# Performance work log

Hardware: AMD Instinct MI355X
Metric: run time of the kernel (lower is better)

The kernel has to match this reference:

```python
import jax, jax.numpy as jnp
import numpy as np

EMBED_DIM = 1024
NUM_HEADS = 16
HEAD_DIM = EMBED_DIM // NUM_HEADS
SCALE = HEAD_DIM ** -0.5


def setup_inputs() -> dict:
    key = jax.random.key(0)
    k_x, k_wqkv, k_bqkv, k_wp, k_bp = jax.random.split(key, 5)
    B, N = 2, 2048
    x = jax.random.normal(k_x, (B, N, EMBED_DIM), dtype=jnp.float32)
    # torch.nn.Linear default init: U(-1/sqrt(fan_in), 1/sqrt(fan_in))
    lim = 1.0 / np.sqrt(EMBED_DIM)
    W_qkv = jax.random.uniform(k_wqkv, (EMBED_DIM, 3 * EMBED_DIM), jnp.float32, -lim, lim)
    b_qkv = jax.random.uniform(k_bqkv, (3 * EMBED_DIM,), jnp.float32, -lim, lim)
    W_proj = jax.random.uniform(k_wp, (EMBED_DIM, EMBED_DIM), jnp.float32, -lim, lim)
    b_proj = jax.random.uniform(k_bp, (EMBED_DIM,), jnp.float32, -lim, lim)
    return {"x": x, "W_qkv": W_qkv, "b_qkv": b_qkv, "W_proj": W_proj, "b_proj": b_proj}


def reference(x, W_qkv, b_qkv, W_proj, b_proj):
    B, N, C = x.shape
    qkv = x @ W_qkv + b_qkv                              # [B, N, 3C]
    qkv = qkv.reshape(B, N, 3, NUM_HEADS, HEAD_DIM)
    qkv = jnp.transpose(qkv, (2, 0, 3, 1, 4))            # [3, B, H, N, D]
    q, k, v = qkv[0], qkv[1], qkv[2]
    attn = jnp.einsum('bhnd,bhmd->bhnm', q, k) * SCALE   # [B, H, N, N]
    attn = jax.nn.softmax(attn, axis=-1)
    out = jnp.einsum('bhnm,bhmd->bhnd', attn, v)         # [B, H, N, D]
    out = jnp.transpose(out, (0, 2, 1, 3)).reshape(B, N, C)
    return out @ W_proj + b_proj
```

## Files before the change

### kernel.cpp

```cpp
#include <hip/hip_runtime.h>
#include <math.h>

typedef unsigned short u16;
typedef _Float16 f16;
typedef f16 f16x8 __attribute__((ext_vector_type(8)));
typedef __fp16 hp16x2 __attribute__((ext_vector_type(2)));
typedef float f32x4 __attribute__((ext_vector_type(4)));
typedef float f32x16 __attribute__((ext_vector_type(16)));
typedef unsigned u32x2 __attribute__((ext_vector_type(2)));

#define SEQ   2048
#define NH    16
#define HD    64
#define EMB   1024
#define NQKV  3072
#define BATCH 2
#define QSCALE 0.18033688f

__device__ __forceinline__ u16 f2h(float f) {
  union { f16 h; u16 u; } w; w.h = (f16)f; return w.u;
}

__device__ __forceinline__ void gload16(const void* g, void* l) {
  __builtin_amdgcn_global_load_lds(
      (const __attribute__((address_space(1))) unsigned int*)g,
      (__attribute__((address_space(3))) unsigned int*)l, 16, 0, 0);
}

__device__ __forceinline__ void cvt_wt_tile(const float* __restrict__ W,
                                            u16* __restrict__ Wt,
                                            int K, int N, int n0, int k0, int t) {
  __shared__ u16 T[64][68];
  const int rr = t >> 4, cc = (t & 15) << 2;
#pragma unroll
  for (int p = 0; p < 4; p++) {
    const int kr = p * 16 + rr;
    float4 v = *reinterpret_cast<const float4*>(&W[(size_t)(k0 + kr) * N + n0 + cc]);
    T[cc + 0][kr] = f2h(v.x); T[cc + 1][kr] = f2h(v.y);
    T[cc + 2][kr] = f2h(v.z); T[cc + 3][kr] = f2h(v.w);
  }
  __syncthreads();
#pragma unroll
  for (int p = 0; p < 4; p++) {
    const int nr = p * 16 + rr;
    union { u16 s[4]; unsigned long long d; } o;
    o.s[0] = T[nr][cc + 0]; o.s[1] = T[nr][cc + 1];
    o.s[2] = T[nr][cc + 2]; o.s[3] = T[nr][cc + 3];
    *reinterpret_cast<unsigned long long*>(&Wt[(size_t)(n0 + nr) * K + k0 + cc]) = o.d;
  }
}

__global__ __launch_bounds__(256) void k_pre(const float* __restrict__ X,
                                             u16* __restrict__ Xh,
                                             const float* __restrict__ Wqkv,
                                             u16* __restrict__ Wt,
                                             const float* __restrict__ Wproj,
                                             u16* __restrict__ Wpt) {
  const int b = blockIdx.x;
  const int t = threadIdx.x;
  if (b < 2048) {
    const size_t i = ((size_t)b * 256 + t) * 8;
    float4 a = *reinterpret_cast<const float4*>(&X[i]);
    float4 c = *reinterpret_cast<const float4*>(&X[i + 4]);
    union { hp16x2 h2[4]; float4 f; } pk;
    pk.h2[0] = __builtin_amdgcn_cvt_pkrtz(a.x, a.y);
    pk.h2[1] = __builtin_amdgcn_cvt_pkrtz(a.z, a.w);
    pk.h2[2] = __builtin_amdgcn_cvt_pkrtz(c.x, c.y);
    pk.h2[3] = __builtin_amdgcn_cvt_pkrtz(c.z, c.w);
    *reinterpret_cast<float4*>(&Xh[i]) = pk.f;
  } else if (b < 2048 + 768) {
    const int id = b - 2048;
    cvt_wt_tile(Wqkv, Wt, EMB, NQKV, (id % 48) << 6, (id / 48) << 6, t);
  } else {
    const int id = b - 2816;
    cvt_wt_tile(Wproj, Wpt, EMB, EMB, (id % 16) << 6, (id / 16) << 6, t);
  }
}

__device__ __forceinline__ void gemm_core_sb(const u16* __restrict__ Ag,
                                             const u16* __restrict__ Bg,
                                             int m0, int n0, int t,
                                             f32x4 acc[4][4]) {
  __shared__ __align__(16) u16 As[128 * 32];
  __shared__ __align__(16) u16 Bs[128 * 32];
  const int lane = t & 63, w = t >> 6;
  const int l15  = lane & 15, quad = lane >> 4;
  const int wm = w >> 1, wn = w & 1;
  const int srow  = lane >> 2;
  const int gslot = (lane & 3) ^ ((srow >> 1) & 3);
  const int xk    = (quad ^ ((l15 >> 1) & 3)) << 3;

  for (int k0 = 0; k0 < EMB; k0 += 32) {
    __syncthreads();
#pragma unroll
    for (int i = 0; i < 2; i++) {
      const int ca = w * 2 + i;
      const int arow = ca * 16 + srow;
      gload16(Ag + (size_t)(m0 + arow) * EMB + k0 + gslot * 8, &As[ca * 512]);
      gload16(Bg + (size_t)(n0 + arow) * EMB + k0 + gslot * 8, &Bs[ca * 512]);
    }
    __syncthreads();
    f16x8 af[4], bf[4];
#pragma unroll
    for (int s = 0; s < 4; s++)
      af[s] = *reinterpret_cast<const f16x8*>(&As[(wm * 64 + s * 16 + l15) * 32 + xk]);
#pragma unroll
    for (int s = 0; s < 4; s++)
      bf[s] = *reinterpret_cast<const f16x8*>(&Bs[(wn * 64 + s * 16 + l15) * 32 + xk]);
#pragma unroll
    for (int i = 0; i < 4; i++)
#pragma unroll
      for (int j = 0; j < 4; j++)
        acc[i][j] = __builtin_amdgcn_mfma_f32_16x16x32_f16(af[i], bf[j], acc[i][j], 0, 0, 0);
  }
}

__global__ __launch_bounds__(128, 2) void k_qkv(const u16* __restrict__ Ag,
                                                const u16* __restrict__ Bg,
                                                const float* __restrict__ bias,
                                                u16* __restrict__ qo,
                                                u16* __restrict__ ko,
                                                u16* __restrict__ vo) {
  __shared__ __align__(16) u16 SM[4][128 * 32];
  const int t = threadIdx.x;
  const int lane = t & 63, w = t >> 6;
  const int l15 = lane & 15, quad = lane >> 4;
  const int srow  = lane >> 2;
  const int gslot = (lane & 3) ^ ((srow >> 1) & 3);
  const int xk    = (quad ^ ((l15 >> 1) & 3)) << 3;
  const int id  = blockIdx.y * 24 + blockIdx.x;
  const int xcd = id & 7, rr = id >> 3;
  const int n_t = 12 * (xcd & 1) + rr % 12;
  const int m_t = 8 * (xcd >> 1) + rr / 12;
  const int m0 = m_t << 7, n0 = n_t << 7;

  f32x4 acc[4][8];
#pragma unroll
  for (int i = 0; i < 4; i++)
#pragma unroll
    for (int j = 0; j < 8; j++) acc[i][j] = (f32x4){0.f, 0.f, 0.f, 0.f};

  auto STAGE = [&](int buf, int k0) {
#pragma unroll
    for (int i = 0; i < 4; i++) {
      const int ca = w * 4 + i;
      const int arow = ca * 16 + srow;
      gload16(Ag + (size_t)(m0 + arow) * EMB + k0 + gslot * 8, &SM[buf][ca * 512]);
      gload16(Bg + (size_t)(n0 + arow) * EMB + k0 + gslot * 8, &SM[2 + buf][ca * 512]);
    }
  };

  STAGE(0, 0);
  __syncthreads();

  for (int kt = 0; kt < 32; ++kt) {
    if (kt + 1 < 32) STAGE((kt + 1) & 1, (kt + 1) * 32);
    const u16* Asb = SM[kt & 1];
    const u16* Bsb = SM[2 + (kt & 1)];
    f16x8 af[4], bf[8];
#pragma unroll
    for (int s = 0; s < 4; s++)
      af[s] = *reinterpret_cast<const f16x8*>(
          &Asb[(w * 64 + s * 16 + l15) * 32 + xk]);
#pragma unroll
    for (int s = 0; s < 8; s++)
      bf[s] = *reinterpret_cast<const f16x8*>(
          &Bsb[(s * 16 + l15) * 32 + xk]);
    __builtin_amdgcn_s_setprio(1);
#pragma unroll
    for (int i = 0; i < 4; i++)
#pragma unroll
      for (int j = 0; j < 8; j++)
        acc[i][j] = __builtin_amdgcn_mfma_f32_16x16x32_f16(af[i], bf[j],
                                                           acc[i][j], 0, 0, 0);
    __builtin_amdgcn_s_setprio(0);
    __syncthreads();
  }

  if (n0 >= 2048) {
    u16* T = &SM[0][0];
#pragma unroll
    for (int j = 0; j < 8; j++) {
      const int c  = n0 + j * 16 + l15;
      const float bv = bias[c];
      const int dl = j * 16 + l15;
#pragma unroll
      for (int i = 0; i < 4; i++) {
#pragma unroll
        for (int r2 = 0; r2 < 4; r2++) {
          const int ml = w * 64 + i * 16 + quad * 4 + r2;
          T[dl * 128 + ((((ml >> 3) ^ (dl & 15)) << 3) | (ml & 7))] =
              f2h(acc[i][j][r2] + bv);
        }
      }
    }
    __syncthreads();
    const int bb = m0 >> 11, nb = m0 & (SEQ - 1);
    const int cg = lane & 15;
#pragma unroll
    for (int it = 0; it < 16; ++it) {
      const int row = w * 64 + it * 4 + (lane >> 4);
      union { f16x8 v; float4 f; } u;
      u.v = *reinterpret_cast<const f16x8*>(
          &T[row * 128 + ((cg ^ (row & 15)) << 3)]);
      const int c = n0 + row;
      const int h = (c >> 6) & 15, d = c & 63;
      *reinterpret_cast<float4*>(
          &vo[((size_t)(bb * NH + h) * HD + d) * SEQ + nb + cg * 8]) = u.f;
    }
  } else {
#pragma unroll
    for (int j = 0; j < 8; j++) {
      const int c = n0 + j * 16 + l15;
      const int which = c >> 10, h = (c >> 6) & 15, d = c & 63;
      const float bv = bias[c];
      const float sc = (which == 0) ? QSCALE : 1.0f;
#pragma unroll
      for (int i = 0; i < 4; i++) {
#pragma unroll
        for (int r2 = 0; r2 < 4; r2++) {
          const int m  = m0 + w * 64 + i * 16 + quad * 4 + r2;
          const int bb = m >> 11, n = m & (SEQ - 1);
          const u16 val = f2h((acc[i][j][r2] + bv) * sc);
          if (which == 1)
            ko[((((size_t)bb * NH + h) * SEQ) + n) * HD + d] = val;
          else
            qo[((((size_t)bb * NH + h) * SEQ) + n) * HD + d] = val;
        }
      }
    }
  }
}

__global__ __launch_bounds__(256) void k_proj(const u16* __restrict__ Ag,
                                              const u16* __restrict__ Bg,
                                              const float* __restrict__ bias,
                                              float* __restrict__ out) {
  const int t = threadIdx.x;
  const int lane = t & 63, w = t >> 6;
  const int l15 = lane & 15, quad = lane >> 4;
  const int wm = w >> 1, wn = w & 1;
  const int m0 = blockIdx.y << 7, n0 = blockIdx.x << 7;
  f32x4 acc[4][4];
#pragma unroll
  for (int i = 0; i < 4; i++)
#pragma unroll
    for (int j = 0; j < 4; j++) acc[i][j] = (f32x4){0.f, 0.f, 0.f, 0.f};
  gemm_core_sb(Ag, Bg, m0, n0, t, acc);
#pragma unroll
  for (int j = 0; j < 4; j++) {
    const int c = n0 + wn * 64 + j * 16 + l15;
    const float bv = bias[c];
#pragma unroll
    for (int i = 0; i < 4; i++) {
#pragma unroll
      for (int r2 = 0; r2 < 4; r2++) {
        const int m = m0 + wm * 64 + i * 16 + quad * 4 + r2;
        out[(size_t)m * EMB + c] = acc[i][j][r2] + bv;
      }
    }
  }
}

__global__ __launch_bounds__(512, 4) void k_attn(const u16* __restrict__ Qg,
                                                 const u16* __restrict__ Kg,
                                                 const u16* __restrict__ Vtg,
                                                 u16* __restrict__ AO) {
  __shared__ __align__(16) u16 KV[2][2][2][64 * 64];
  __shared__ float Lx[256];
  const int t    = threadIdx.x;
  const int lane = t & 63, w = t >> 6;
  const int grp  = w >> 2, wl = w & 3;
  const int l31  = lane & 31, hi = lane >> 5;
  const int id   = blockIdx.y * 16 + blockIdx.x;
  const int swz  = ((id & 7) << 6) | (id >> 3);
  const int bh   = swz >> 4;
  const int q0   = (swz & 15) << 7;
  const size_t base = (size_t)bh * SEQ * HD;

  f16x8 qf[4];
  {
    const u16* qp = Qg + base + (size_t)(q0 + 32 * wl + l31) * HD + hi * 8;
#pragma unroll
    for (int c = 0; c < 4; c++) {
      union { float4 f; f16x8 v; } fu;
      fu.f = *reinterpret_cast<const float4*>(qp + c * 16);
      qf[c] = fu.v;
    }
  }

  f32x16 O0 = {}, O1 = {};
  float lsum = 0.f;
  const int fsw = (l31 >> 1) & 7;
  const int srw = lane >> 3, ssl = lane & 7;
  const int kbeg = grp << 10;
  const int kend = kbeg + (SEQ / 2);

  auto STAGE = [&](int buf, int kt) {
    u16* Ksb = KV[buf][grp][0];
    u16* Vsb = KV[buf][grp][1];
#pragma unroll
    for (int i = 0; i < 2; i++) {
      const int ca  = wl * 2 + i;
      const int row = ca * 8 + srw;
      const int sg  = (ssl ^ ((row >> 1) & 7)) << 3;
      gload16(Kg  + base + (size_t)(kt + row) * HD + sg, &Ksb[ca * 512]);
      gload16(Vtg + base + (size_t)row * SEQ + kt + sg,  &Vsb[ca * 512]);
    }
  };

  STAGE(0, kbeg);
  __syncthreads();

  int cur = 0;
  for (int kt = kbeg; kt < kend; kt += 64) {
    if (kt + 64 < kend) STAGE(cur ^ 1, kt + 64);
    const u16* Ks = KV[cur][grp][0];
    const u16* Vs = KV[cur][grp][1];

#pragma unroll
    for (int sk = 0; sk < 2; sk++) {
      f32x16 c = {};
      __builtin_amdgcn_s_setprio(1);
#pragma unroll
      for (int cc = 0; cc < 4; cc++) {
        f16x8 kf = *reinterpret_cast<const f16x8*>(
            &Ks[(sk * 32 + l31) * 64 + (((cc * 2 + hi) ^ fsw) << 3)]);
        c = __builtin_amdgcn_mfma_f32_32x32x16_f16(kf, qf[cc], c, 0, 0, 0);
      }
      __builtin_amdgcn_s_setprio(0);
      unsigned pw[4][2];
#pragma unroll
      for (int g = 0; g < 4; g++) {
        const float p0 = __builtin_amdgcn_exp2f(c[4 * g + 0]);
        const float p1 = __builtin_amdgcn_exp2f(c[4 * g + 1]);
        const float p2 = __builtin_amdgcn_exp2f(c[4 * g + 2]);
        const float p3 = __builtin_amdgcn_exp2f(c[4 * g + 3]);
        lsum += (p0 + p1) + (p2 + p3);
        union { hp16x2 h; unsigned u; } w0, w1;
        w0.h = __builtin_amdgcn_cvt_pkrtz(p0, p1);
        w1.h = __builtin_amdgcn_cvt_pkrtz(p2, p3);
        pw[g][0] = w0.u; pw[g][1] = w1.u;
      }
      __builtin_amdgcn_s_setprio(1);
#pragma unroll
      for (int s = 0; s < 2; s++) {
        u32x2 r02 = __builtin_amdgcn_permlane32_swap(
            pw[2 * s][0], pw[2 * s + 1][0], false, false);
        u32x2 r13 = __builtin_amdgcn_permlane32_swap(
            pw[2 * s][1], pw[2 * s + 1][1], false, false);
        union { unsigned u[4]; f16x8 v; } fr;
        fr.u[0] = r02.x;
        fr.u[1] = r13.x;
        fr.u[2] = r02.y;
        fr.u[3] = r13.y;
        const int cc = sk * 2 + s;
        f16x8 vf0 = *reinterpret_cast<const f16x8*>(
            &Vs[l31 * 64 + (((cc * 2 + hi) ^ fsw) << 3)]);
        f16x8 vf1 = *reinterpret_cast<const f16x8*>(
            &Vs[(32 + l31) * 64 + (((cc * 2 + hi) ^ fsw) << 3)]);
        O0 = __builtin_amdgcn_mfma_f32_32x32x16_f16(fr.v, vf0, O0, 0, 0, 0);
        O1 = __builtin_amdgcn_mfma_f32_32x32x16_f16(fr.v, vf1, O1, 0, 0, 0);
      }
      __builtin_amdgcn_s_setprio(0);
    }
    __syncthreads();
    cur ^= 1;
  }

  float* Xch = reinterpret_cast<float*>(&KV[0][0][0][0]);
  const int li = wl * 64 + lane;
  if (grp == 1) {
#pragma unroll
    for (int g4 = 0; g4 < 4; g4++) {
      f32x4 v0 = { O0[4 * g4 + 0], O0[4 * g4 + 1], O0[4 * g4 + 2], O0[4 * g4 + 3] };
      *reinterpret_cast<f32x4*>(&Xch[(g4 * 256 + li) * 4]) = v0;
      f32x4 v1 = { O1[4 * g4 + 0], O1[4 * g4 + 1], O1[4 * g4 + 2], O1[4 * g4 + 3] };
      *reinterpret_cast<f32x4*>(&Xch[((4 + g4) * 256 + li) * 4]) = v1;
    }
    Lx[li] = lsum;
  }
  __syncthreads();
  if (grp == 0) {
#pragma unroll
    for (int g4 = 0; g4 < 4; g4++) {
      f32x4 v0 = *reinterpret_cast<const f32x4*>(&Xch[(g4 * 256 + li) * 4]);
      f32x4 v1 = *reinterpret_cast<const f32x4*>(&Xch[((4 + g4) * 256 + li) * 4]);
#pragma unroll
      for (int j = 0; j < 4; j++) {
        O0[4 * g4 + j] += v0[j];
        O1[4 * g4 + j] += v1[j];
      }
    }
    lsum += Lx[li];
    lsum += __shfl_xor(lsum, 32);
    const int b = bh >> 4, h = bh & 15;
#pragma unroll
    for (int g = 0; g < 4; g++) {
#pragma unroll
      for (int rr = 0; rr < 4; rr++) {
        const int r = g * 4 + rr;
        const int qrow = rr + 8 * g + 4 * hi;
        const float inv = 1.f / __shfl(lsum, qrow, 64);
        const int n = q0 + 32 * wl + qrow;
        u16* dst = AO + ((size_t)(b * SEQ + n)) * EMB + h * HD;
        dst[l31]      = f2h(O0[r] * inv);
        dst[32 + l31] = f2h(O1[r] * inv);
      }
    }
  }
}

extern "C" void kernel_launch(void* const* d_in, const int* in_sizes, int n_in,
                              void* d_out, int out_size, void* d_ws, size_t ws_size,
                              hipStream_t stream) {
  (void)in_sizes; (void)n_in; (void)out_size; (void)ws_size;
  const float* x     = (const float*)d_in[0];
  const float* Wqkv  = (const float*)d_in[1];
  const float* bqkv  = (const float*)d_in[2];
  const float* Wproj = (const float*)d_in[3];
  const float* bproj = (const float*)d_in[4];
  float* out = (float*)d_out;

  const size_t NE = (size_t)BATCH * SEQ * EMB;
  u16* q    = (u16*)d_ws;
  u16* k    = q + NE;
  u16* vt   = k + NE;
  u16* aoxh = vt + NE;
  u16* Wt   = aoxh + NE;
  u16* Wpt  = Wt + (size_t)NQKV * EMB;

  k_pre<<<3072, 256, 0, stream>>>(x, aoxh, Wqkv, Wt, Wproj, Wpt);

  dim3 gq(NQKV / 128, (BATCH * SEQ) / 128);
  k_qkv<<<gq, 128, 0, stream>>>(aoxh, Wt, bqkv, q, k, vt);

  dim3 ga(SEQ / 128, BATCH * NH);
  k_attn<<<ga, 512, 0, stream>>>(q, k, vt, aoxh);

  dim3 gp(EMB / 128, (BATCH * SEQ) / 128);
  k_proj<<<gp, 256, 0, stream>>>(aoxh, Wpt, bproj, out);
}
```

Measured before the change: 187.2 us.

## Give each attention wave two 32-row query tiles, halving block size

```diff
diff --git a/kernel.cpp b/kernel.cpp
--- a/kernel.cpp
+++ b/kernel.cpp
@@ -262,15 +262,15 @@
   }
 }
 
-__global__ __launch_bounds__(512, 4) void k_attn(const u16* __restrict__ Qg,
-                                                 const u16* __restrict__ Kg,
-                                                 const u16* __restrict__ Vtg,
-                                                 u16* __restrict__ AO) {
+__global__ __launch_bounds__(256) void k_attn(const u16* __restrict__ Qg,
+                                              const u16* __restrict__ Kg,
+                                              const u16* __restrict__ Vtg,
+                                              u16* __restrict__ AO) {
   __shared__ __align__(16) u16 KV[2][2][2][64 * 64];
-  __shared__ float Lx[256];
+  __shared__ float Lx[2][128];
   const int t    = threadIdx.x;
   const int lane = t & 63, w = t >> 6;
-  const int grp  = w >> 2, wl = w & 3;
+  const int grp  = w >> 1, wl = w & 1;
   const int l31  = lane & 31, hi = lane >> 5;
   const int id   = blockIdx.y * 16 + blockIdx.x;
   const int swz  = ((id & 7) << 6) | (id >> 3);
@@ -278,19 +278,20 @@
   const int q0   = (swz & 15) << 7;
   const size_t base = (size_t)bh * SEQ * HD;
 
-  f16x8 qf[4];
-  {
-    const u16* qp = Qg + base + (size_t)(q0 + 32 * wl + l31) * HD + hi * 8;
+  f16x8 qf[2][4];
+#pragma unroll
+  for (int qs = 0; qs < 2; qs++) {
+    const u16* qp = Qg + base + (size_t)(q0 + 64 * wl + 32 * qs + l31) * HD + hi * 8;
 #pragma unroll
     for (int c = 0; c < 4; c++) {
       union { float4 f; f16x8 v; } fu;
       fu.f = *reinterpret_cast<const float4*>(qp + c * 16);
-      qf[c] = fu.v;
-    }
-  }
-
-  f32x16 O0 = {}, O1 = {};
-  float lsum = 0.f;
+      qf[qs][c] = fu.v;
+    }
+  }
+
+  f32x16 O[2][2] = {};
+  float lsum[2] = {0.f, 0.f};
   const int fsw = (l31 >> 1) & 7;
   const int srw = lane >> 3, ssl = lane & 7;
   const int kbeg = grp << 10;
@@ -300,8 +301,8 @@
     u16* Ksb = KV[buf][grp][0];
     u16* Vsb = KV[buf][grp][1];
 #pragma unroll
-    for (int i = 0; i < 2; i++) {
-      const int ca  = wl * 2 + i;
+    for (int i = 0; i < 4; i++) {
+      const int ca  = wl * 4 + i;
       const int row = ca * 8 + srw;
       const int sg  = (ssl ^ ((row >> 1) & 7)) << 3;
       gload16(Kg  + base + (size_t)(kt + row) * HD + sg, &Ksb[ca * 512]);
@@ -320,47 +321,54 @@
 
 #pragma unroll
     for (int sk = 0; sk < 2; sk++) {
-      f32x16 c = {};
+      f32x16 cq[2] = {};
       __builtin_amdgcn_s_setprio(1);
 #pragma unroll
       for (int cc = 0; cc < 4; cc++) {
         f16x8 kf = *reinterpret_cast<const f16x8*>(
             &Ks[(sk * 32 + l31) * 64 + (((cc * 2 + hi) ^ fsw) << 3)]);
-        c = __builtin_amdgcn_mfma_f32_32x32x16_f16(kf, qf[cc], c, 0, 0, 0);
+        cq[0] = __builtin_amdgcn_mfma_f32_32x32x16_f16(kf, qf[0][cc], cq[0], 0, 0, 0);
+        cq[1] = __builtin_amdgcn_mfma_f32_32x32x16_f16(kf, qf[1][cc], cq[1], 0, 0, 0);
       }
       __builtin_amdgcn_s_setprio(0);
-      unsigned pw[4][2];
-#pragma unroll
-      for (int g = 0; g < 4; g++) {
-        const float p0 = __builtin_amdgcn_exp2f(c[4 * g + 0]);
-        const float p1 = __builtin_amdgcn_exp2f(c[4 * g + 1]);
-        const float p2 = __builtin_amdgcn_exp2f(c[4 * g + 2]);
-        const float p3 = __builtin_amdgcn_exp2f(c[4 * g + 3]);
-        lsum += (p0 + p1) + (p2 + p3);
-        union { hp16x2 h; unsigned u; } w0, w1;
-        w0.h = __builtin_amdgcn_cvt_pkrtz(p0, p1);
-        w1.h = __builtin_amdgcn_cvt_pkrtz(p2, p3);
-        pw[g][0] = w0.u; pw[g][1] = w1.u;
+      unsigned pw[2][4][2];
+#pragma unroll
+      for (int qs = 0; qs < 2; qs++) {
+#pragma unroll
+        for (int g = 0; g < 4; g++) {
+          const float p0 = __builtin_amdgcn_exp2f(cq[qs][4 * g + 0]);
+          const float p1 = __builtin_amdgcn_exp2f(cq[qs][4 * g + 1]);
+          const float p2 = __builtin_amdgcn_exp2f(cq[qs][4 * g + 2]);
+          const float p3 = __builtin_amdgcn_exp2f(cq[qs][4 * g + 3]);
+          lsum[qs] += (p0 + p1) + (p2 + p3);
+          union { hp16x2 h; unsigned u; } w0, w1;
+          w0.h = __builtin_amdgcn_cvt_pkrtz(p0, p1);
+          w1.h = __builtin_amdgcn_cvt_pkrtz(p2, p3);
+          pw[qs][g][0] = w0.u; pw[qs][g][1] = w1.u;
+        }
       }
       __builtin_amdgcn_s_setprio(1);
 #pragma unroll
       for (int s = 0; s < 2; s++) {
-        u32x2 r02 = __builtin_amdgcn_permlane32_swap(
-            pw[2 * s][0], pw[2 * s + 1][0], false, false);
-        u32x2 r13 = __builtin_amdgcn_permlane32_swap(
-            pw[2 * s][1], pw[2 * s + 1][1], false, false);
-        union { unsigned u[4]; f16x8 v; } fr;
-        fr.u[0] = r02.x;
-        fr.u[1] = r13.x;
-        fr.u[2] = r02.y;
-        fr.u[3] = r13.y;
         const int cc = sk * 2 + s;
         f16x8 vf0 = *reinterpret_cast<const f16x8*>(
             &Vs[l31 * 64 + (((cc * 2 + hi) ^ fsw) << 3)]);
         f16x8 vf1 = *reinterpret_cast<const f16x8*>(
             &Vs[(32 + l31) * 64 + (((cc * 2 + hi) ^ fsw) << 3)]);
-        O0 = __builtin_amdgcn_mfma_f32_32x32x16_f16(fr.v, vf0, O0, 0, 0, 0);
-        O1 = __builtin_amdgcn_mfma_f32_32x32x16_f16(fr.v, vf1, O1, 0, 0, 0);
+#pragma unroll
+        for (int qs = 0; qs < 2; qs++) {
+          u32x2 r02 = __builtin_amdgcn_permlane32_swap(
+              pw[qs][2 * s][0], pw[qs][2 * s + 1][0], false, false);
+          u32x2 r13 = __builtin_amdgcn_permlane32_swap(
+              pw[qs][2 * s][1], pw[qs][2 * s + 1][1], false, false);
+          union { unsigned u[4]; f16x8 v; } fr;
+          fr.u[0] = r02.x;
+          fr.u[1] = r13.x;
+          fr.u[2] = r02.y;
+          fr.u[3] = r13.y;
+          O[qs][0] = __builtin_amdgcn_mfma_f32_32x32x16_f16(fr.v, vf0, O[qs][0], 0, 0, 0);
+          O[qs][1] = __builtin_amdgcn_mfma_f32_32x32x16_f16(fr.v, vf1, O[qs][1], 0, 0, 0);
+        }
       }
       __builtin_amdgcn_s_setprio(0);
     }
@@ -372,40 +380,51 @@
   const int li = wl * 64 + lane;
   if (grp == 1) {
 #pragma unroll
-    for (int g4 = 0; g4 < 4; g4++) {
-      f32x4 v0 = { O0[4 * g4 + 0], O0[4 * g4 + 1], O0[4 * g4 + 2], O0[4 * g4 + 3] };
-      *reinterpret_cast<f32x4*>(&Xch[(g4 * 256 + li) * 4]) = v0;
-      f32x4 v1 = { O1[4 * g4 + 0], O1[4 * g4 + 1], O1[4 * g4 + 2], O1[4 * g4 + 3] };
-      *reinterpret_cast<f32x4*>(&Xch[((4 + g4) * 256 + li) * 4]) = v1;
-    }
-    Lx[li] = lsum;
+    for (int qs = 0; qs < 2; qs++)
+#pragma unroll
+      for (int half = 0; half < 2; half++)
+#pragma unroll
+        for (int g4 = 0; g4 < 4; g4++) {
+          f32x4 v = { O[qs][half][4 * g4 + 0], O[qs][half][4 * g4 + 1],
+                      O[qs][half][4 * g4 + 2], O[qs][half][4 * g4 + 3] };
+          *reinterpret_cast<f32x4*>(
+              &Xch[(((qs * 2 + half) * 4 + g4) * 128 + li) * 4]) = v;
+        }
+    Lx[0][li] = lsum[0];
+    Lx[1][li] = lsum[1];
   }
   __syncthreads();
   if (grp == 0) {
 #pragma unroll
-    for (int g4 = 0; g4 < 4; g4++) {
-      f32x4 v0 = *reinterpret_cast<const f32x4*>(&Xch[(g4 * 256 + li) * 4]);
-      f32x4 v1 = *reinterpret_cast<const f32x4*>(&Xch[((4 + g4) * 256 + li) * 4]);
-#pragma unroll
-      for (int j = 0; j < 4; j++) {
-        O0[4 * g4 + j] += v0[j];
-        O1[4 * g4 + j] += v1[j];
-      }
-    }
-    lsum += Lx[li];
-    lsum += __shfl_xor(lsum, 32);
+    for (int qs = 0; qs < 2; qs++)
+#pragma unroll
+      for (int half = 0; half < 2; half++)
+#pragma unroll
+        for (int g4 = 0; g4 < 4; g4++) {
+          f32x4 v = *reinterpret_cast<const f32x4*>(
+              &Xch[(((qs * 2 + half) * 4 + g4) * 128 + li) * 4]);
+#pragma unroll
+          for (int j = 0; j < 4; j++) O[qs][half][4 * g4 + j] += v[j];
+        }
+    lsum[0] += Lx[0][li];
+    lsum[1] += Lx[1][li];
+    lsum[0] += __shfl_xor(lsum[0], 32);
+    lsum[1] += __shfl_xor(lsum[1], 32);
     const int b = bh >> 4, h = bh & 15;
 #pragma unroll
-    for (int g = 0; g < 4; g++) {
-#pragma unroll
-      for (int rr = 0; rr < 4; rr++) {
-        const int r = g * 4 + rr;
-        const int qrow = rr + 8 * g + 4 * hi;
-        const float inv = 1.f / __shfl(lsum, qrow, 64);
-        const int n = q0 + 32 * wl + qrow;
-        u16* dst = AO + ((size_t)(b * SEQ + n)) * EMB + h * HD;
-        dst[l31]      = f2h(O0[r] * inv);
-        dst[32 + l31] = f2h(O1[r] * inv);
+    for (int qs = 0; qs < 2; qs++) {
+#pragma unroll
+      for (int g = 0; g < 4; g++) {
+#pragma unroll
+        for (int rr = 0; rr < 4; rr++) {
+          const int r = g * 4 + rr;
+          const int qrow = rr + 8 * g + 4 * hi;
+          const float inv = 1.f / __shfl(lsum[qs], qrow, 64);
+          const int n = q0 + 64 * wl + 32 * qs + qrow;
+          u16* dst = AO + ((size_t)(b * SEQ + n)) * EMB + h * HD;
+          dst[l31]      = f2h(O[qs][0][r] * inv);
+          dst[32 + l31] = f2h(O[qs][1][r] * inv);
+        }
       }
     }
   }
@@ -436,7 +455,7 @@
   k_qkv<<<gq, 128, 0, stream>>>(aoxh, Wt, bqkv, q, k, vt);
 
   dim3 ga(SEQ / 128, BATCH * NH);
-  k_attn<<<ga, 512, 0, stream>>>(q, k, vt, aoxh);
+  k_attn<<<ga, 256, 0, stream>>>(q, k, vt, aoxh);
 
   dim3 gp(EMB / 128, (BATCH * SEQ) / 128);
   k_proj<<<gp, 256, 0, stream>>>(aoxh, Wpt, bproj, out);
```

New measurement: 189.8 us. No clear change (+1.4%).
